# Performance work log

Hardware: AMD Instinct MI355X
Metric: run time of the kernel (lower is better)

Reference implementation:

```python
import jax, jax.numpy as jnp
import numpy as np

B, D, K = 65536, 512, 64
H1, H2 = 256, 128
START_TEMP, MIN_TEMP, NR_EPOCHS = 10.0, 0.1, 1000


def setup_inputs() -> dict:
    key = jax.random.key(0)
    ks = jax.random.split(key, 12)
    x = jax.random.normal(ks[0], (B, D), dtype=jnp.float32)
    label = jax.random.normal(ks[1], (B, 1), dtype=jnp.float32)
    u = jax.random.uniform(ks[2], (B, K), dtype=jnp.float32, minval=1e-6, maxval=1.0)
    # MLP params: D -> H1 -> H2 -> K (relu on hidden layers, bias everywhere)
    W1 = jax.random.normal(ks[3], (D, H1), dtype=jnp.float32) / np.sqrt(D)
    b1 = jnp.zeros((H1,), dtype=jnp.float32)
    W2 = jax.random.normal(ks[4], (H1, H2), dtype=jnp.float32) / np.sqrt(H1)
    b2 = jnp.zeros((H2,), dtype=jnp.float32)
    W3 = jax.random.normal(ks[5], (H2, K), dtype=jnp.float32) / np.sqrt(H2)
    b3 = jnp.zeros((K,), dtype=jnp.float32)
    # thetas ~ Uniform(0,1) per torch init.uniform_
    thetas = jax.random.uniform(ks[6], (D, K), dtype=jnp.float32)
    return {"x": x, "label": label, "u": u, "W1": W1, "b1": b1,
            "W2": W2, "b2": b2, "W3": W3, "b3": b3,
            "thetas": thetas, "epoch": 100}


def _current_temp(epoch):
    # exponential schedule: max(min_temp, start*(min/start)**(epoch/nr_epochs))
    t = START_TEMP * (MIN_TEMP / START_TEMP) ** (epoch / NR_EPOCHS)
    return jnp.maximum(jnp.float32(MIN_TEMP), jnp.float32(t))


def reference(x, label, u, W1, b1, W2, b2, W3, b3, thetas, epoch):
    # MLP -> logits [B, K]
    h = jax.nn.relu(x @ W1 + b1)
    h = jax.nn.relu(h @ W2 + b2)
    logits = h @ W3 + b3
    # Concrete (Gumbel-softmax) feature selection over the K candidate predictors
    xt = x @ thetas                      # [B, K]
    gumbel = -jnp.log(-jnp.log(u))
    temp = _current_temp(jnp.float32(epoch))
    weights = jax.nn.softmax((logits + gumbel) / temp, axis=1)
    # diagonal(xt @ weights.T) == row-wise dot product (O(B*K), not O(B^2*K))
    selected = jnp.sum(xt * weights, axis=1, keepdims=True)  # [B, 1]
    loss = jnp.mean((selected - label) ** 2)
    return loss
```

## Files before the change

kernel.cpp:

```cpp
#include <hip/hip_runtime.h>
#include <math.h>

#define Bn  65536
#define Dn  512
#define Kn  64
#define H1n 256
#define H2n 128
#define BM  64

typedef short bf16x8 __attribute__((ext_vector_type(8)));
typedef float floatx4 __attribute__((ext_vector_type(4)));

__device__ __forceinline__ unsigned short f2bf(float f) {
    unsigned u = __builtin_bit_cast(unsigned, f);
    u += 0x7FFF + ((u >> 16) & 1);
    return (unsigned short)(u >> 16);
}

__device__ __forceinline__ unsigned cvt_pk_bf16(float lo, float hi) {
    unsigned r;
    asm("v_cvt_pk_bf16_f32 %0, %1, %2" : "=v"(r) : "v"(lo), "v"(hi));
    return r;
}

__global__ __launch_bounds__(256)
void prep_k(const float* __restrict__ W1, const float* __restrict__ W2,
            const float* __restrict__ W3, const float* __restrict__ Th,
            unsigned short* __restrict__ ws)
{
    const int gid = blockIdx.x * 256 + threadIdx.x;
    if (gid < 131072) {
        const int s = gid, k = s >> 8, n = s & 255;
        const int dst = (((n >> 4) * 16 + (k >> 5)) * 64 + ((k >> 3) & 3) * 16 + (n & 15)) * 8 + (k & 7);
        ws[dst] = f2bf(W1[s]);
    } else if (gid < 163840) {
        const int s = gid - 131072, k = s >> 6, n = s & 63;
        const int dst = 131072 + (((n >> 4) * 16 + (k >> 5)) * 64 + ((k >> 3) & 3) * 16 + (n & 15)) * 8 + (k & 7);
        ws[dst] = f2bf(Th[s]);
    } else if (gid < 196608) {
        const int s = gid - 163840, k = s >> 7, n = s & 127;
        const int dst = 163840 + (((n >> 4) * 8 + (k >> 5)) * 64 + ((k >> 3) & 3) * 16 + (n & 15)) * 8 + (k & 7);
        ws[dst] = f2bf(W2[s]);
    } else if (gid < 204800) {
        const int s = gid - 196608, k = s >> 6, n = s & 63;
        const int dst = 196608 + (((n >> 4) * 4 + (k >> 5)) * 64 + ((k >> 3) & 3) * 16 + (n & 15)) * 8 + (k & 7);
        ws[dst] = f2bf(W3[s]);
    }
}

__global__ __launch_bounds__(1024)
void reduce_k(const float* __restrict__ p, float* __restrict__ out)
{
    __shared__ float sred[16];
    const int tid = threadIdx.x;
    float s = 0.f;
    #pragma unroll
    for (int i = 0; i < 8; ++i) s += p[tid + i * 1024];
    #pragma unroll
    for (int off = 32; off > 0; off >>= 1) s += __shfl_xor(s, off);
    if ((tid & 63) == 0) sred[tid >> 6] = s;
    __syncthreads();
    if (tid < 64) {
        float v = (tid < 16) ? sred[tid] : 0.f;
        #pragma unroll
        for (int off = 8; off > 0; off >>= 1) v += __shfl_xor(v, off);
        if (tid == 0) out[0] = v * (1.0f / (float)Bn);
    }
}

__global__ __launch_bounds__(512)
__attribute__((amdgpu_waves_per_eu(4, 4)))
void llp_mfma(const float* __restrict__ x,
              const float* __restrict__ label,
              const float* __restrict__ u,
              const float* __restrict__ b1, const float* __restrict__ b2,
              const float* __restrict__ b3,
              const unsigned short* __restrict__ W1f,
              const unsigned short* __restrict__ Tf,
              const unsigned short* __restrict__ W2f,
              const unsigned short* __restrict__ W3f,
              const int* __restrict__ epoch_p,
              float* __restrict__ partials)
{
    __shared__ char smem[65536];

    const int tid  = threadIdx.x;
    const int row0 = blockIdx.x * BM;
    const int w    = tid >> 6;
    const int lane = tid & 63;
    const int lrow = lane & 15;
    const int quad = lane >> 4;

    {
        const float4* xg4 = (const float4*)(x + (size_t)row0 * Dn);
        #pragma unroll
        for (int i = 0; i < 16; ++i) {
            const int f = tid + i * 512;
            const float4 v = xg4[f];
            const int row = f >> 7, c4 = f & 127;
            const int kb = c4 >> 1, half = c4 & 1;
            uint2 o2;
            o2.x = cvt_pk_bf16(v.x, v.y);
            o2.y = cvt_pk_bf16(v.z, v.w);
            *(uint2*)(smem + ((row * 64 + (kb ^ (row & 7))) << 4) + (half << 3)) = o2;
        }
    }

    const int ct0  = w * 2;
    const int ct_x = w & 3;
    const int rt_a = (w >> 2) * 2;
    bf16x8 aB[4], bB[2][2], bT[2];
    #pragma unroll
    for (int t = 0; t < 2; ++t)
        bB[0][t] = *(const bf16x8*)(W1f + ((((ct0 + t) * 16 + 0) * 64 + lane) << 3));
    bT[0] = *(const bf16x8*)(Tf + (((ct_x * 16 + 0) * 64 + lane) << 3));
    __syncthreads();

    floatx4 acc[4][2], accT[2];
    #pragma unroll
    for (int t = 0; t < 2; ++t) {
        const float bv = b1[(ct0 + t) * 16 + lrow];
        #pragma unroll
        for (int rt = 0; rt < 4; ++rt) acc[rt][t] = (floatx4){bv, bv, bv, bv};
    }
    accT[0] = (floatx4){0.f, 0.f, 0.f, 0.f};
    accT[1] = (floatx4){0.f, 0.f, 0.f, 0.f};

#define P1_LOOP(XT0, XT1)                                                            \
    _Pragma("unroll")                                                                \
    for (int ks = 0; ks < 16; ++ks) {                                                \
        const int cur = ks & 1, nxt = cur ^ 1;                                       \
        if (ks < 15) {          \
            const int kn = ks + 1;                                                   \
            _Pragma("unroll")                                                        \
            for (int t = 0; t < 2; ++t)                                              \
                bB[nxt][t] = *(const bf16x8*)(W1f + ((((ct0 + t) * 16 + kn) * 64 + lane) << 3)); \
            bT[nxt] = *(const bf16x8*)(Tf + (((ct_x * 16 + kn) * 64 + lane) << 3));  \
        }                                                                            \
        _Pragma("unroll")                 \
        for (int rt = 0; rt < 4; ++rt)                                               \
            aB[rt] = *(const bf16x8*)(smem +                                         \
                (((rt * 16 + lrow) * 64 + ((ks * 4 + quad) ^ (lrow & 7))) << 4));    \
        _Pragma("unroll")                                                            \
        for (int rt = 0; rt < 4; ++rt)                                               \
            _Pragma("unroll")                                                        \
            for (int t = 0; t < 2; ++t)                                              \
                acc[rt][t] = __builtin_amdgcn_mfma_f32_16x16x32_bf16(aB[rt], bB[cur][t], acc[rt][t], 0, 0, 0); \
        accT[0] = __builtin_amdgcn_mfma_f32_16x16x32_bf16(aB[XT0], bT[cur], accT[0], 0, 0, 0); \
        accT[1] = __builtin_amdgcn_mfma_f32_16x16x32_bf16(aB[XT1], bT[cur], accT[1], 0, 0, 0); \
    }

    if (rt_a == 0) { P1_LOOP(0, 1) } else { P1_LOOP(2, 3) }
#undef P1_LOOP

    __syncthreads();

    #pragma unroll
    for (int rt = 0; rt < 4; ++rt) {
        #pragma unroll
        for (int t = 0; t < 2; ++t) {
            const int col = (ct0 + t) * 16 + lrow;
            #pragma unroll
            for (int g = 0; g < 4; ++g) {
                const int orow = rt * 16 + quad * 4 + g;
                *(unsigned short*)(smem +
                    ((orow * 32 + ((col >> 3) ^ (orow & 7))) << 4) + ((col & 7) << 1))
                    = f2bf(fmaxf(acc[rt][t][g], 0.0f));
            }
        }
    }
    {
        float* xtf = (float*)(smem + 32768);
        const int xcol = (ct_x * 16 + lrow) ^ (quad << 4);
        #pragma unroll
        for (int r = 0; r < 2; ++r)
            #pragma unroll
            for (int g = 0; g < 4; ++g)
                xtf[((rt_a + r) * 16 + quad * 4 + g) * 64 + xcol] = accT[r][g];
    }

    bf16x8 a2[4], b2B[2];
    b2B[0] = *(const bf16x8*)(W2f + (((w * 8 + 0) * 64 + lane) << 3));
    float upf[8], labpf[8];
    #pragma unroll
    for (int rr = 0; rr < 8; ++rr) {
        upf[rr]   = u[(size_t)(row0 + w * 8 + rr) * Kn + lane];
        labpf[rr] = label[row0 + w * 8 + rr];
    }
    __syncthreads();

    floatx4 acc2[4];
    {
        const float bv = b2[w * 16 + lrow];
        #pragma unroll
        for (int rt = 0; rt < 4; ++rt) acc2[rt] = (floatx4){bv, bv, bv, bv};
    }
    #pragma unroll
    for (int ks = 0; ks < 8; ++ks) {
        const int cur = ks & 1, nxt = cur ^ 1;
        if (ks < 7)
            b2B[nxt] = *(const bf16x8*)(W2f + (((w * 8 + ks + 1) * 64 + lane) << 3));
        #pragma unroll
        for (int rt = 0; rt < 4; ++rt)
            a2[rt] = *(const bf16x8*)(smem +
                (((rt * 16 + lrow) * 32 + ((ks * 4 + quad) ^ (lrow & 7))) << 4));
        #pragma unroll
        for (int rt = 0; rt < 4; ++rt)
            acc2[rt] = __builtin_amdgcn_mfma_f32_16x16x32_bf16(a2[rt], b2B[cur], acc2[rt], 0, 0, 0);
    }
    #pragma unroll
    for (int rt = 0; rt < 4; ++rt) {
        const int col = w * 16 + lrow;
        #pragma unroll
        for (int g = 0; g < 4; ++g) {
            const int orow = rt * 16 + quad * 4 + g;
            *(unsigned short*)(smem + 49152 +
                ((orow * 16 + ((col >> 3) ^ (orow & 7))) << 4) + ((col & 7) << 1))
                = f2bf(fmaxf(acc2[rt][g], 0.0f));
        }
    }

    const int ct3 = w & 3;
    const int rt3 = (w >> 2) * 2;
    bf16x8 bb[4];
    #pragma unroll
    for (int ks = 0; ks < 4; ++ks)
        bb[ks] = *(const bf16x8*)(W3f + (((ct3 * 4 + ks) * 64 + lane) << 3));
    __syncthreads();

    floatx4 acc3[2];
    {
        const float bv = b3[ct3 * 16 + lrow];
        acc3[0] = (floatx4){bv, bv, bv, bv};
        acc3[1] = (floatx4){bv, bv, bv, bv};
    }
    {
        bf16x8 aa[2][4];
        #pragma unroll
        for (int ks = 0; ks < 4; ++ks)
            #pragma unroll
            for (int r = 0; r < 2; ++r) {
                const int row = (rt3 + r) * 16 + lrow;
                aa[r][ks] = *(const bf16x8*)(smem + 49152 +
                    ((row * 16 + ((ks * 4 + quad) ^ (row & 7))) << 4));
            }
        #pragma unroll
        for (int ks = 0; ks < 4; ++ks)
            #pragma unroll
            for (int r = 0; r < 2; ++r)
                acc3[r] = __builtin_amdgcn_mfma_f32_16x16x32_bf16(aa[r][ks], bb[ks], acc3[r], 0, 0, 0);
    }
    {
        float* lgf = (float*)smem;
        const int xcol = (ct3 * 16 + lrow) ^ (quad << 4);
        #pragma unroll
        for (int r = 0; r < 2; ++r)
            #pragma unroll
            for (int g = 0; g < 4; ++g)
                lgf[((rt3 + r) * 16 + quad * 4 + g) * 64 + xcol] = acc3[r][g];
    }
    __syncthreads();

    {
        const float* lgf = (const float*)smem;
        const float* xtf = (const float*)(smem + 32768);
        const int ep = *epoch_p;
        const float tmp = 10.0f * powf(0.01f, (float)ep * 0.001f);
        const float inv_temp = 1.0f / fmaxf(0.1f, tmp);

        float partial = 0.0f;
        #pragma unroll
        for (int rr = 0; rr < 8; ++rr) {
            const int rw = w * 8 + rr;
            const int rlane = lane ^ ((rw & 12) << 2);
            const float g = -logf(-logf(upf[rr]));
            float s = (lgf[rw * 64 + rlane] + g) * inv_temp;
            float m = s;
            #pragma unroll
            for (int off = 32; off > 0; off >>= 1)
                m = fmaxf(m, __shfl_xor(m, off));
            const float e = expf(s - m);
            float sum = e;
            float ws_ = e * xtf[rw * 64 + rlane];
            #pragma unroll
            for (int off = 32; off > 0; off >>= 1) {
                sum += __shfl_xor(sum, off);
                ws_ += __shfl_xor(ws_, off);
            }
            const float diff = ws_ / sum - labpf[rr];
            partial = fmaf(diff, diff, partial);
        }
        if (lane == 0)
            partials[blockIdx.x * 8 + w] = partial;
    }
}

extern "C" void kernel_launch(void* const* d_in, const int* in_sizes, int n_in,
                              void* d_out, int out_size, void* d_ws, size_t ws_size,
                              hipStream_t stream) {
    const float* x      = (const float*)d_in[0];
    const float* label  = (const float*)d_in[1];
    const float* u      = (const float*)d_in[2];
    const float* W1     = (const float*)d_in[3];
    const float* b1     = (const float*)d_in[4];
    const float* W2     = (const float*)d_in[5];
    const float* b2     = (const float*)d_in[6];
    const float* W3     = (const float*)d_in[7];
    const float* b3     = (const float*)d_in[8];
    const float* thetas = (const float*)d_in[9];
    const int*   epoch  = (const int*)d_in[10];
    float* out = (float*)d_out;

    unsigned short* wsb = (unsigned short*)d_ws;
    float* partials = (float*)((char*)d_ws + 409600);

    prep_k<<<800, 256, 0, stream>>>(W1, W2, W3, thetas, wsb);
    llp_mfma<<<Bn / BM, 512, 0, stream>>>(x, label, u, b1, b2, b3,
                                          wsb, wsb + 131072, wsb + 163840, wsb + 196608,
                                          epoch, partials);
    reduce_k<<<1, 1024, 0, stream>>>(partials, out);
}
```

Before: 257.3 us.

## Triple-buffer weight prefetch with inline-asm loads and explicit vmcnt waits

Replaces the double-buffered compiler loads of W1/Theta and W2 fragments with inline-asm global_load_dwordx4 issued two k-steps ahead into a three-slot ring. Explicit s_waitcnt vmcnt and sched_barrier calls control when data is awaited, aiming to hide global-load latency behind the MFMA chains. Bias loads are hoisted to kernel start, and the u/label prefetch moves after the layer-2 GEMM. The layer-1 and layer-2 __syncthreads are replaced by lgkmcnt waits plus s_barrier. Because the compiler does not track the asm loads, its own vmcnt accounting may be wrong, so correctness relies on the manual wait counts.

Result: faster. 248.8 us (-3.3%).

```diff
diff --git a/kernel.cpp b/kernel.cpp
--- a/kernel.cpp
+++ b/kernel.cpp
@@ -22,6 +22,9 @@
     asm("v_cvt_pk_bf16_f32 %0, %1, %2" : "=v"(r) : "v"(lo), "v"(hi));
     return r;
 }
+
+#define GLOAD(dst, ptr) \
+    asm volatile("global_load_dwordx4 %0, %1, off" : "=v"(dst) : "v"(ptr))
 
 __global__ __launch_bounds__(256)
 void prep_k(const float* __restrict__ W1, const float* __restrict__ W2,
@@ -91,6 +94,17 @@
     const int lrow = lane & 15;
     const int quad = lane >> 4;
 
+    const int ct0  = w * 2;
+    const int ct_x = w & 3;
+    const int rt_a = (w >> 2) * 2;
+    const int ct3  = w & 3;
+    const int rt3  = (w >> 2) * 2;
+
+    const float b1v0 = b1[(ct0 + 0) * 16 + lrow];
+    const float b1v1 = b1[(ct0 + 1) * 16 + lrow];
+    const float b2v  = b2[w * 16 + lrow];
+    const float b3v  = b3[ct3 * 16 + lrow];
+
     {
         const float4* xg4 = (const float4*)(x + (size_t)row0 * Dn);
         #pragma unroll
@@ -106,48 +120,52 @@
         }
     }
 
-    const int ct0  = w * 2;
-    const int ct_x = w & 3;
-    const int rt_a = (w >> 2) * 2;
-    bf16x8 aB[4], bB[2][2], bT[2];
-    #pragma unroll
-    for (int t = 0; t < 2; ++t)
-        bB[0][t] = *(const bf16x8*)(W1f + ((((ct0 + t) * 16 + 0) * 64 + lane) << 3));
-    bT[0] = *(const bf16x8*)(Tf + (((ct_x * 16 + 0) * 64 + lane) << 3));
-    __syncthreads();
-
     floatx4 acc[4][2], accT[2];
     #pragma unroll
-    for (int t = 0; t < 2; ++t) {
-        const float bv = b1[(ct0 + t) * 16 + lrow];
-        #pragma unroll
-        for (int rt = 0; rt < 4; ++rt) acc[rt][t] = (floatx4){bv, bv, bv, bv};
+    for (int rt = 0; rt < 4; ++rt) {
+        acc[rt][0] = (floatx4){b1v0, b1v0, b1v0, b1v0};
+        acc[rt][1] = (floatx4){b1v1, b1v1, b1v1, b1v1};
     }
     accT[0] = (floatx4){0.f, 0.f, 0.f, 0.f};
     accT[1] = (floatx4){0.f, 0.f, 0.f, 0.f};
+
+    bf16x8 aB[4], bB[3][2], bT[3];
+    GLOAD(bB[0][0], W1f + ((((ct0 + 0) * 16 + 0) * 64 + lane) << 3));
+    GLOAD(bB[0][1], W1f + ((((ct0 + 1) * 16 + 0) * 64 + lane) << 3));
+    GLOAD(bT[0],    Tf  + (((ct_x * 16 + 0) * 64 + lane) << 3));
+    GLOAD(bB[1][0], W1f + ((((ct0 + 0) * 16 + 1) * 64 + lane) << 3));
+    GLOAD(bB[1][1], W1f + ((((ct0 + 1) * 16 + 1) * 64 + lane) << 3));
+    GLOAD(bT[1],    Tf  + (((ct_x * 16 + 1) * 64 + lane) << 3));
+
+    asm volatile("s_waitcnt lgkmcnt(0)" ::: "memory");
+    __builtin_amdgcn_s_barrier();
 
 #define P1_LOOP(XT0, XT1)                                                            \
     _Pragma("unroll")                                                                \
     for (int ks = 0; ks < 16; ++ks) {                                                \
-        const int cur = ks & 1, nxt = cur ^ 1;                                       \
-        if (ks < 15) {          \
-            const int kn = ks + 1;                                                   \
-            _Pragma("unroll")                                                        \
-            for (int t = 0; t < 2; ++t)                                              \
-                bB[nxt][t] = *(const bf16x8*)(W1f + ((((ct0 + t) * 16 + kn) * 64 + lane) << 3)); \
-            bT[nxt] = *(const bf16x8*)(Tf + (((ct_x * 16 + kn) * 64 + lane) << 3));  \
+        const int wsl = ks % 3;                                                      \
+        if (ks < 14) {            \
+            const int kn = ks + 2, sl = kn % 3;                                      \
+            GLOAD(bB[sl][0], W1f + ((((ct0 + 0) * 16 + kn) * 64 + lane) << 3));      \
+            GLOAD(bB[sl][1], W1f + ((((ct0 + 1) * 16 + kn) * 64 + lane) << 3));      \
+            GLOAD(bT[sl],    Tf  + (((ct_x * 16 + kn) * 64 + lane) << 3));           \
         }                                                                            \
-        _Pragma("unroll")                 \
+        __builtin_amdgcn_sched_barrier(0);                                           \
+        _Pragma("unroll")        \
         for (int rt = 0; rt < 4; ++rt)                                               \
             aB[rt] = *(const bf16x8*)(smem +                                         \
                 (((rt * 16 + lrow) * 64 + ((ks * 4 + quad) ^ (lrow & 7))) << 4));    \
+        if (ks < 14)      { asm volatile("s_waitcnt vmcnt(6)" ::: "memory"); }       \
+        else if (ks == 14){ asm volatile("s_waitcnt vmcnt(3)" ::: "memory"); }       \
+        else              { asm volatile("s_waitcnt vmcnt(0)" ::: "memory"); }       \
+        __builtin_amdgcn_sched_barrier(0);                                           \
         _Pragma("unroll")                                                            \
-        for (int rt = 0; rt < 4; ++rt)                                               \
-            _Pragma("unroll")                                                        \
-            for (int t = 0; t < 2; ++t)                                              \
-                acc[rt][t] = __builtin_amdgcn_mfma_f32_16x16x32_bf16(aB[rt], bB[cur][t], acc[rt][t], 0, 0, 0); \
-        accT[0] = __builtin_amdgcn_mfma_f32_16x16x32_bf16(aB[XT0], bT[cur], accT[0], 0, 0, 0); \
-        accT[1] = __builtin_amdgcn_mfma_f32_16x16x32_bf16(aB[XT1], bT[cur], accT[1], 0, 0, 0); \
+        for (int rt = 0; rt < 4; ++rt) {                                             \
+            acc[rt][0] = __builtin_amdgcn_mfma_f32_16x16x32_bf16(aB[rt], bB[wsl][0], acc[rt][0], 0, 0, 0); \
+            acc[rt][1] = __builtin_amdgcn_mfma_f32_16x16x32_bf16(aB[rt], bB[wsl][1], acc[rt][1], 0, 0, 0); \
+        }                                                                            \
+        accT[0] = __builtin_amdgcn_mfma_f32_16x16x32_bf16(aB[XT0], bT[wsl], accT[0], 0, 0, 0); \
+        accT[1] = __builtin_amdgcn_mfma_f32_16x16x32_bf16(aB[XT1], bT[wsl], accT[1], 0, 0, 0); \
     }
 
     if (rt_a == 0) { P1_LOOP(0, 1) } else { P1_LOOP(2, 3) }
@@ -179,35 +197,44 @@
                 xtf[((rt_a + r) * 16 + quad * 4 + g) * 64 + xcol] = accT[r][g];
     }
 
-    bf16x8 a2[4], b2B[2];
-    b2B[0] = *(const bf16x8*)(W2f + (((w * 8 + 0) * 64 + lane) << 3));
+    floatx4 acc2[4];
+    #pragma unroll
+    for (int rt = 0; rt < 4; ++rt) acc2[rt] = (floatx4){b2v, b2v, b2v, b2v};
+    bf16x8 a2[4], b2B[3];
+    GLOAD(b2B[0], W2f + (((w * 8 + 0) * 64 + lane) << 3));
+    GLOAD(b2B[1], W2f + (((w * 8 + 1) * 64 + lane) << 3));
+
+    asm volatile("s_waitcnt lgkmcnt(0)" ::: "memory");
+    __builtin_amdgcn_s_barrier();
+
+    #pragma unroll
+    for (int ks = 0; ks < 8; ++ks) {
+        const int wsl = ks % 3;
+        if (ks < 6) {
+            const int kn = ks + 2, sl = kn % 3;
+            GLOAD(b2B[sl], W2f + (((w * 8 + kn) * 64 + lane) << 3));
+        }
+        __builtin_amdgcn_sched_barrier(0);
+        #pragma unroll
+        for (int rt = 0; rt < 4; ++rt)
+            a2[rt] = *(const bf16x8*)(smem +
+                (((rt * 16 + lrow) * 32 + ((ks * 4 + quad) ^ (lrow & 7))) << 4));
+        if (ks < 6)      { asm volatile("s_waitcnt vmcnt(2)" ::: "memory"); }
+        else if (ks == 6){ asm volatile("s_waitcnt vmcnt(1)" ::: "memory"); }
+        else             { asm volatile("s_waitcnt vmcnt(0)" ::: "memory"); }
+        __builtin_amdgcn_sched_barrier(0);
+        #pragma unroll
+        for (int rt = 0; rt < 4; ++rt)
+            acc2[rt] = __builtin_amdgcn_mfma_f32_16x16x32_bf16(a2[rt], b2B[wsl], acc2[rt], 0, 0, 0);
+    }
+
     float upf[8], labpf[8];
     #pragma unroll
     for (int rr = 0; rr < 8; ++rr) {
         upf[rr]   = u[(size_t)(row0 + w * 8 + rr) * Kn + lane];
         labpf[rr] = label[row0 + w * 8 + rr];
     }
-    __syncthreads();
-
-    floatx4 acc2[4];
-    {
-        const float bv = b2[w * 16 + lrow];
-        #pragma unroll
-        for (int rt = 0; rt < 4; ++rt) acc2[rt] = (floatx4){bv, bv, bv, bv};
-    }
-    #pragma unroll
-    for (int ks = 0; ks < 8; ++ks) {
-        const int cur = ks & 1, nxt = cur ^ 1;
-        if (ks < 7)
-            b2B[nxt] = *(const bf16x8*)(W2f + (((w * 8 + ks + 1) * 64 + lane) << 3));
-        #pragma unroll
-        for (int rt = 0; rt < 4; ++rt)
-            a2[rt] = *(const bf16x8*)(smem +
-                (((rt * 16 + lrow) * 32 + ((ks * 4 + quad) ^ (lrow & 7))) << 4));
-        #pragma unroll
-        for (int rt = 0; rt < 4; ++rt)
-            acc2[rt] = __builtin_amdgcn_mfma_f32_16x16x32_bf16(a2[rt], b2B[cur], acc2[rt], 0, 0, 0);
-    }
+
     #pragma unroll
     for (int rt = 0; rt < 4; ++rt) {
         const int col = w * 16 + lrow;
@@ -220,8 +247,6 @@
         }
     }
 
-    const int ct3 = w & 3;
-    const int rt3 = (w >> 2) * 2;
     bf16x8 bb[4];
     #pragma unroll
     for (int ks = 0; ks < 4; ++ks)
@@ -229,11 +254,8 @@
     __syncthreads();
 
     floatx4 acc3[2];
-    {
-        const float bv = b3[ct3 * 16 + lrow];
-        acc3[0] = (floatx4){bv, bv, bv, bv};
-        acc3[1] = (floatx4){bv, bv, bv, bv};
-    }
+    acc3[0] = (floatx4){b3v, b3v, b3v, b3v};
+    acc3[1] = (floatx4){b3v, b3v, b3v, b3v};
     {
         bf16x8 aa[2][4];
         #pragma unroll
```
